# Optimization experiments

Measured on AMD Instinct MI355X. Metric: run time of the kernel, lower is better.

The kernel has to match this reference:

```python
import jax, jax.numpy as jnp
import numpy as np

N_NODES = 50000
N_EDGES = 600000
N_FEAT = 128
NHID = 128
N_CLASSES = 10
N_GRAPHS = 512
BN_EPS = 1e-5


def _gcn_conv(x, W, b, src, dst, n):
    """PyG GCNConv: D^{-1/2}(A+I)D^{-1/2} X W + b (symmetric norm, self-loops)."""
    xw = x @ W  # [n, out]
    deg = jax.ops.segment_sum(jnp.ones(src.shape[0], x.dtype), dst, num_segments=n) + 1.0
    dinv = jax.lax.rsqrt(deg)  # [n]
    norm = dinv[src] * dinv[dst]  # [E]
    agg = jax.ops.segment_sum(xw[src] * norm[:, None], dst, num_segments=n)
    agg = agg + xw * (dinv * dinv)[:, None]  # self-loop contribution
    return agg + b


def setup_inputs() -> dict:
    key = jax.random.key(0)
    ks = jax.random.split(key, 16)
    s_in = 1.0 / np.sqrt(N_FEAT)
    s_h = 1.0 / np.sqrt(NHID)
    s_h2 = 1.0 / np.sqrt(NHID // 2)
    return {
        "x": jax.random.normal(ks[0], (N_NODES, N_FEAT), jnp.float32),
        "edge_index": jax.random.randint(ks[1], (2, N_EDGES), 0, N_NODES, jnp.int32),
        "batch": jnp.sort(jax.random.randint(ks[2], (N_NODES,), 0, N_GRAPHS, jnp.int32)),
        "W1": jax.random.normal(ks[3], (N_FEAT, NHID), jnp.float32) * s_in,
        "b1": jnp.zeros((NHID,), jnp.float32),
        "W2": jax.random.normal(ks[4], (NHID, NHID), jnp.float32) * s_h,
        "b2": jnp.zeros((NHID,), jnp.float32),
        "W3": jax.random.normal(ks[5], (NHID, NHID), jnp.float32) * s_h,
        "b3": jnp.zeros((NHID,), jnp.float32),
        "gamma": jnp.ones((NHID,), jnp.float32),
        "beta": jnp.zeros((NHID,), jnp.float32),
        "run_mean": jnp.zeros((NHID,), jnp.float32),
        "run_var": jnp.ones((NHID,), jnp.float32),
        "lw1": jax.random.normal(ks[6], (NHID, NHID), jnp.float32) * s_h,
        "lb1": jnp.zeros((NHID,), jnp.float32),
        "lw2": jax.random.normal(ks[7], (NHID, NHID // 2), jnp.float32) * s_h,
        "lb2": jnp.zeros((NHID // 2,), jnp.float32),
        "lw3": jax.random.normal(ks[8], (NHID // 2, N_CLASSES), jnp.float32) * s_h2,
        "lb3": jnp.zeros((N_CLASSES,), jnp.float32),
    }


def reference(x, edge_index, batch, W1, b1, W2, b2, W3, b3,
              gamma, beta, run_mean, run_var,
              lw1, lb1, lw2, lb2, lw3, lb3):
    src, dst = edge_index[0], edge_index[1]
    h = jax.nn.relu(_gcn_conv(x, W1, b1, src, dst, N_NODES))
    h = jax.nn.relu(_gcn_conv(h, W2, b2, src, dst, N_NODES))
    h = jax.nn.relu(_gcn_conv(h, W3, b3, src, dst, N_NODES))
    # BatchNorm1d (eval: running stats)
    h = (h - run_mean) * jax.lax.rsqrt(run_var + BN_EPS) * gamma + beta
    # scatter_max over graph ids -> [N_GRAPHS, NHID]
    g = jax.ops.segment_max(h, batch, num_segments=N_GRAPHS)
    g = jax.nn.relu(g @ lw1 + lb1)
    g = jax.nn.relu(g @ lw2 + lb2)
    return g @ lw3 + lb3
```

## Files before the change

kernel.cpp:

```cpp
#include <hip/hip_runtime.h>
#include <hip/hip_bf16.h>

#define NHID 128
#define NGRAPH 512
#define NCLS 10

typedef __attribute__((ext_vector_type(8))) short bf16x8;
typedef __attribute__((ext_vector_type(4))) float f32x4;
typedef __attribute__((ext_vector_type(4))) unsigned int u32x4;

__device__ inline unsigned int fenc(float f) {
    unsigned int u = __float_as_uint(f);
    return (u & 0x80000000u) ? ~u : (u | 0x80000000u);
}
__device__ inline float fdec(unsigned int u) {
    u = (u & 0x80000000u) ? (u & 0x7fffffffu) : ~u;
    return __uint_as_float(u);
}
__device__ inline unsigned short f2bf(float f) {
    unsigned int u = __float_as_uint(f);
    return (unsigned short)((u + 0x7fffu + ((u >> 16) & 1u)) >> 16);
}
__device__ inline unsigned int packbf(float lo, float hi) {
    return (unsigned)f2bf(lo) | ((unsigned)f2bf(hi) << 16);
}

__global__ void k_deg(const int* __restrict__ dst, int* __restrict__ cnt, int E) {
    int e = blockIdx.x * blockDim.x + threadIdx.x;
    if (e < E) atomicAdd(&cnt[dst[e]], 1);
}

__global__ __launch_bounds__(1024) void k_scan1(const int* __restrict__ cnt,
        float* __restrict__ dinv, int* __restrict__ rowptr,
        int* __restrict__ bsum, int N) {
    __shared__ int lds[1024];
    int t = threadIdx.x;
    int i = blockIdx.x * 1024 + t;
    int v = (i < N) ? cnt[i] : 0;
    if (i < N) dinv[i] = rsqrtf((float)v + 1.0f);
    lds[t] = v;
    __syncthreads();
    for (int off = 1; off < 1024; off <<= 1) {
        int x = (t >= off) ? lds[t - off] : 0;
        __syncthreads();
        lds[t] += x;
        __syncthreads();
    }
    if (i < N) rowptr[i + 1] = lds[t];
    if (t == 1023) bsum[blockIdx.x] = lds[1023];
}

__global__ __launch_bounds__(1024) void k_scan2(int* __restrict__ bsum, int nb) {
    __shared__ int lds[1024];
    int t = threadIdx.x;
    int v = (t < nb) ? bsum[t] : 0;
    lds[t] = v;
    __syncthreads();
    for (int off = 1; off < 1024; off <<= 1) {
        int x = (t >= off) ? lds[t - off] : 0;
        __syncthreads();
        lds[t] += x;
        __syncthreads();
    }
    if (t < nb) bsum[t] = lds[t] - v;
}

__global__ void k_scan3(int* __restrict__ rowptr, const int* __restrict__ bsum, int N) {
    int i = blockIdx.x * 256 + threadIdx.x;
    if (i < N) rowptr[i + 1] += bsum[i >> 10];
    if (i == 0) rowptr[0] = 0;
}

__global__ void k_fill(const int* __restrict__ src, const int* __restrict__ dst,
                       const float* __restrict__ dinv, const int* __restrict__ rowptr,
                       int* __restrict__ cursor, int2* __restrict__ csr, int E) {
    int e = blockIdx.x * blockDim.x + threadIdx.x;
    if (e >= E) return;
    int s = src[e], d = dst[e];
    int pos = rowptr[d] + atomicAdd(&cursor[d], 1);
    csr[pos] = make_int2(s, __float_as_int(dinv[s] * dinv[d]));
}

__global__ void k_prep(const float* __restrict__ x, unsigned int* __restrict__ xb, int n8,
                       const float* __restrict__ W1, const float* __restrict__ W2,
                       const float* __restrict__ W3, unsigned short* __restrict__ Wt) {
    int i = blockIdx.x * 256 + threadIdx.x;
    if (i < n8) {
        const float* p = x + (size_t)i * 8;
        f32x4 a = *reinterpret_cast<const f32x4*>(p);
        f32x4 b = *reinterpret_cast<const f32x4*>(p + 4);
        u32x4 o;
        o[0] = packbf(a[0], a[1]);
        o[1] = packbf(a[2], a[3]);
        o[2] = packbf(b[0], b[1]);
        o[3] = packbf(b[2], b[3]);
        *reinterpret_cast<u32x4*>(xb + (size_t)i * 4) = o;
    } else {
        int idx = i - n8;
        if (idx < 3 * 16384) {
            int l = idx >> 14;
            int r = idx & 16383;
            const float* W = (l == 0) ? W1 : (l == 1) ? W2 : W3;
            int c = r & 127, k = r >> 7;
            Wt[l * 16384 + c * NHID + k] = f2bf(W[k * NHID + c]);
        }
    }
}

__device__ inline void fma8(const u32x4& u, float nw, float* a) {
#pragma unroll
    for (int q = 0; q < 4; ++q) {
        a[2 * q]     = fmaf(nw, __uint_as_float(u[q] << 16), a[2 * q]);
        a[2 * q + 1] = fmaf(nw, __uint_as_float(u[q] & 0xffff0000u), a[2 * q + 1]);
    }
}

__global__ __launch_bounds__(256) void k_agg(const unsigned int* __restrict__ Hb,
        const int2* __restrict__ csr, const int* __restrict__ rowptr,
        const float* __restrict__ dinv, unsigned int* __restrict__ aggb, int N) {
    int w = (blockIdx.x * 256 + threadIdx.x) >> 6;
    if (w >= N) return;
    int lane = threadIdx.x & 63;
    int g = lane >> 4;
    int l16 = lane & 15;
    float di = dinv[w];
    u32x4 us = reinterpret_cast<const u32x4*>(Hb + (size_t)w * (NHID / 2))[l16];
    float a[8];
#pragma unroll
    for (int e = 0; e < 8; ++e) a[e] = 0.f;
    int beg = rowptr[w], end = rowptr[w + 1];
    int trips = (end - beg + 15) >> 4;
    int j = beg + g;
    for (int t = 0; t < trips; ++t, j += 16) {
        int s0 = w, s1 = w, s2 = w, s3 = w;
        float n0 = 0.f, n1 = 0.f, n2 = 0.f, n3 = 0.f;
        if (j < end)      { int2 e2 = csr[j];      s0 = e2.x; n0 = __int_as_float(e2.y); }
        if (j + 4 < end)  { int2 e2 = csr[j + 4];  s1 = e2.x; n1 = __int_as_float(e2.y); }
        if (j + 8 < end)  { int2 e2 = csr[j + 8];  s2 = e2.x; n2 = __int_as_float(e2.y); }
        if (j + 12 < end) { int2 e2 = csr[j + 12]; s3 = e2.x; n3 = __int_as_float(e2.y); }
        u32x4 u0 = reinterpret_cast<const u32x4*>(Hb + (size_t)s0 * (NHID / 2))[l16];
        u32x4 u1 = reinterpret_cast<const u32x4*>(Hb + (size_t)s1 * (NHID / 2))[l16];
        u32x4 u2 = reinterpret_cast<const u32x4*>(Hb + (size_t)s2 * (NHID / 2))[l16];
        u32x4 u3 = reinterpret_cast<const u32x4*>(Hb + (size_t)s3 * (NHID / 2))[l16];
        fma8(u0, n0, a);
        fma8(u1, n1, a);
        fma8(u2, n2, a);
        fma8(u3, n3, a);
    }
    if (g == 0) fma8(us, di * di, a);
#pragma unroll
    for (int e = 0; e < 8; ++e) {
        a[e] += __shfl_xor(a[e], 16);
        a[e] += __shfl_xor(a[e], 32);
    }
    if (g == 0) {
        u32x4 o;
        o[0] = packbf(a[0], a[1]);
        o[1] = packbf(a[2], a[3]);
        o[2] = packbf(a[4], a[5]);
        o[3] = packbf(a[6], a[7]);
        *reinterpret_cast<u32x4*>(aggb + (size_t)w * (NHID / 2) + l16 * 4) = o;
    }
}

__global__ __launch_bounds__(256) void k_gemm(const unsigned short* __restrict__ A,
        const unsigned short* __restrict__ Wt, const float* __restrict__ bias,
        unsigned short* __restrict__ Hb, int M) {
    int wave = threadIdx.x >> 6;
    int lane = threadIdx.x & 63;
    int lr = lane & 15;
    int kq = lane >> 4;
    int r0 = blockIdx.x * 64 + wave * 16;
    f32x4 acc[8];
#pragma unroll
    for (int nt = 0; nt < 8; ++nt) acc[nt] = 0.f;
    int ar = r0 + lr;
    bool arok = ar < M;
#pragma unroll
    for (int kg = 0; kg < 4; ++kg) {
        int kb = kg * 32 + kq * 8;
        bf16x8 af = bf16x8(0);
        if (arok) af = *reinterpret_cast<const bf16x8*>(A + (size_t)ar * NHID + kb);
#pragma unroll
        for (int nt = 0; nt < 8; ++nt) {
            bf16x8 bf = *reinterpret_cast<const bf16x8*>(Wt + (size_t)(nt * 16 + lr) * NHID + kb);
            acc[nt] = __builtin_amdgcn_mfma_f32_16x16x32_bf16(af, bf, acc[nt], 0, 0, 0);
        }
    }
#pragma unroll
    for (int nt = 0; nt < 8; ++nt) {
        int c = nt * 16 + lr;
        float b = bias[c];
#pragma unroll
        for (int e = 0; e < 4; ++e) {
            int r = r0 + kq * 4 + e;
            if (r < M) {
                float v = fmaxf(acc[nt][e] + b, 0.f);
                Hb[(size_t)r * NHID + c] = f2bf(v);
            }
        }
    }
}

__global__ __launch_bounds__(256) void k_gemm_bn(const unsigned short* __restrict__ A,
        const unsigned short* __restrict__ Wt, const float* __restrict__ bias,
        const int* __restrict__ batch, const float* __restrict__ gamma,
        const float* __restrict__ beta, const float* __restrict__ rmean,
        const float* __restrict__ rvar, unsigned int* __restrict__ keys, int M) {
    __shared__ unsigned int smax[64][NHID];
    __shared__ int bseg[64];
    int tid = threadIdx.x;
    int n0 = blockIdx.x * 64;
    for (int i = tid; i < 64 * NHID; i += 256) ((unsigned int*)smax)[i] = 0u;
    if (tid < 64) {
        int r = n0 + tid;
        bseg[tid] = batch[r < M ? r : M - 1];
    }
    int wave = tid >> 6;
    int lane = tid & 63;
    int lr = lane & 15;
    int kq = lane >> 4;
    int r0 = n0 + wave * 16;
    f32x4 acc[8];
#pragma unroll
    for (int nt = 0; nt < 8; ++nt) acc[nt] = 0.f;
    int ar = r0 + lr;
    bool arok = ar < M;
#pragma unroll
    for (int kg = 0; kg < 4; ++kg) {
        int kb = kg * 32 + kq * 8;
        bf16x8 af = bf16x8(0);
        if (arok) af = *reinterpret_cast<const bf16x8*>(A + (size_t)ar * NHID + kb);
#pragma unroll
        for (int nt = 0; nt < 8; ++nt) {
            bf16x8 bf = *reinterpret_cast<const bf16x8*>(Wt + (size_t)(nt * 16 + lr) * NHID + kb);
            acc[nt] = __builtin_amdgcn_mfma_f32_16x16x32_bf16(af, bf, acc[nt], 0, 0, 0);
        }
    }
    __syncthreads();
    int glo = bseg[0];
#pragma unroll
    for (int nt = 0; nt < 8; ++nt) {
        int c = nt * 16 + lr;
        float b = bias[c];
        float sc = gamma[c] * rsqrtf(rvar[c] + 1e-5f);
        float sh = beta[c] - rmean[c] * sc;
#pragma unroll
        for (int e = 0; e < 4; ++e) {
            int rr = wave * 16 + kq * 4 + e;
            if (n0 + rr < M) {
                float v = fmaxf(acc[nt][e] + b, 0.f);
                float y = fmaf(v, sc, sh);
                atomicMax(&smax[bseg[rr] - glo][c], fenc(y));
            }
        }
    }
    __syncthreads();
    int last = M - 1 - n0;
    if (last > 63) last = 63;
    int span = bseg[last] - glo + 1;
    for (int i = tid; i < span * NHID; i += 256) {
        unsigned int v = ((unsigned int*)smax)[i];
        if (v) atomicMax(&keys[(size_t)(glo + (i >> 7)) * NHID + (i & 127)], v);
    }
}

__global__ __launch_bounds__(128) void k_head(const unsigned int* __restrict__ keys,
        const float* __restrict__ lw1, const float* __restrict__ lb1,
        const float* __restrict__ lw2, const float* __restrict__ lb2,
        const float* __restrict__ lw3, const float* __restrict__ lb3,
        float* __restrict__ out) {
    __shared__ float g0[NHID], g1[NHID], g2[64];
    int r = blockIdx.x;
    int t = threadIdx.x;
    unsigned int u = keys[(size_t)r * NHID + t];
    g0[t] = (u == 0u) ? -3.0e38f : fdec(u);
    __syncthreads();
    float acc = lb1[t];
#pragma unroll 8
    for (int k = 0; k < NHID; ++k) acc = fmaf(g0[k], lw1[k * NHID + t], acc);
    g1[t] = fmaxf(acc, 0.f);
    __syncthreads();
    if (t < 64) {
        acc = lb2[t];
#pragma unroll 8
        for (int k = 0; k < NHID; ++k) acc = fmaf(g1[k], lw2[k * 64 + t], acc);
        g2[t] = fmaxf(acc, 0.f);
    }
    __syncthreads();
    if (t < NCLS) {
        acc = lb3[t];
#pragma unroll 8
        for (int k = 0; k < 64; ++k) acc = fmaf(g2[k], lw3[k * NCLS + t], acc);
        out[(size_t)r * NCLS + t] = acc;
    }
}

extern "C" void kernel_launch(void* const* d_in, const int* in_sizes, int n_in,
                              void* d_out, int out_size, void* d_ws, size_t ws_size,
                              hipStream_t stream) {
    const float* x     = (const float*)d_in[0];
    const int*   ei    = (const int*)d_in[1];
    const int*   batch = (const int*)d_in[2];
    const float* W1 = (const float*)d_in[3];
    const float* b1 = (const float*)d_in[4];
    const float* W2 = (const float*)d_in[5];
    const float* b2 = (const float*)d_in[6];
    const float* W3 = (const float*)d_in[7];
    const float* b3 = (const float*)d_in[8];
    const float* gamma = (const float*)d_in[9];
    const float* beta  = (const float*)d_in[10];
    const float* rmean = (const float*)d_in[11];
    const float* rvar  = (const float*)d_in[12];
    const float* lw1 = (const float*)d_in[13];
    const float* lb1 = (const float*)d_in[14];
    const float* lw2 = (const float*)d_in[15];
    const float* lb2 = (const float*)d_in[16];
    const float* lw3 = (const float*)d_in[17];
    const float* lb3 = (const float*)d_in[18];

    const int N = in_sizes[2];
    const int E = in_sizes[1] / 2;
    const int* src = ei;
    const int* dst = ei + E;

    char* ws = (char*)d_ws;
    size_t off = 0;
    auto alloc = [&](size_t bytes) {
        char* p = ws + off;
        off += (bytes + 255) & ~(size_t)255;
        return p;
    };
    int*   cnt     = (int*)  alloc((size_t)N * 8);
    int*   cursor  = cnt + N;
    int*   rowptr  = (int*)  alloc(((size_t)N + 1) * 4);
    int*   bsum    = (int*)  alloc(1024 * 4);
    float* dinv    = (float*)alloc((size_t)N * 4);
    int2*  csr     = (int2*) alloc((size_t)E * 8);
    unsigned int* xb   = (unsigned int*)alloc((size_t)N * NHID * 2);
    unsigned int* aggb = (unsigned int*)alloc((size_t)N * NHID * 2);
    unsigned int* Hb   = (unsigned int*)alloc((size_t)N * NHID * 2);
    unsigned short* Wt = (unsigned short*)alloc((size_t)3 * NHID * NHID * 2);
    unsigned int* keys = (unsigned int*)alloc((size_t)NGRAPH * NHID * 4);
    (void)ws_size; (void)n_in; (void)out_size;

    hipMemsetAsync(cnt, 0, (size_t)N * 8, stream);
    hipMemsetAsync(keys, 0, (size_t)NGRAPH * NHID * 4, stream);

    int eb = (E + 255) / 256;
    int nb1 = (N + 1023) / 1024;
    k_deg<<<eb, 256, 0, stream>>>(dst, cnt, E);
    k_scan1<<<nb1, 1024, 0, stream>>>(cnt, dinv, rowptr, bsum, N);
    k_scan2<<<1, 1024, 0, stream>>>(bsum, nb1);
    k_scan3<<<(N + 255) / 256, 256, 0, stream>>>(rowptr, bsum, N);
    k_fill<<<eb, 256, 0, stream>>>(src, dst, dinv, rowptr, cursor, csr, E);
    int n8 = N * 16;
    k_prep<<<(n8 + 3 * 16384 + 255) / 256, 256, 0, stream>>>(x, xb, n8, W1, W2, W3, Wt);

    int ab = ((size_t)N * 64 + 255) / 256;
    int gb = (N + 63) / 64;
    k_agg<<<ab, 256, 0, stream>>>(xb, csr, rowptr, dinv, aggb, N);
    k_gemm<<<gb, 256, 0, stream>>>((const unsigned short*)aggb, Wt, b1, (unsigned short*)Hb, N);
    k_agg<<<ab, 256, 0, stream>>>(Hb, csr, rowptr, dinv, aggb, N);
    k_gemm<<<gb, 256, 0, stream>>>((const unsigned short*)aggb, Wt + 16384, b2, (unsigned short*)Hb, N);
    k_agg<<<ab, 256, 0, stream>>>(Hb, csr, rowptr, dinv, aggb, N);
    k_gemm_bn<<<gb, 256, 0, stream>>>((const unsigned short*)aggb, Wt + 32768, b3,
                                      batch, gamma, beta, rmean, rvar, keys, N);

    k_head<<<NGRAPH, 128, 0, stream>>>(keys, lw1, lb1, lw2, lb2, lw3, lb3, (float*)d_out);
}
```

Baseline: 249.3 us.

## Split aggregation into feature partitions and fuse front-end prep kernels

Aggregation now splits the 128 features into four 32-feature partitions, each handled by a separate block group. Within a partition a lane loads 4 bytes per edge instead of 16, and blocks are 1024 threads. The goal is better cache locality: each pass gathers a narrower column slice of H, so the working set that must stay in L2/MALL shrinks. The degree count, x bf16 conversion, weight transpose and keys zeroing are merged into one launch, and the separate scan3 pass is removed by adding the block offset at use sites. In exchange, the CSR is re-read four times and loop and index overhead repeats per partition.

```diff
diff --git a/kernel.cpp b/kernel.cpp
--- a/kernel.cpp
+++ b/kernel.cpp
@@ -24,10 +24,42 @@
 __device__ inline unsigned int packbf(float lo, float hi) {
     return (unsigned)f2bf(lo) | ((unsigned)f2bf(hi) << 16);
 }
-
-__global__ void k_deg(const int* __restrict__ dst, int* __restrict__ cnt, int E) {
-    int e = blockIdx.x * blockDim.x + threadIdx.x;
-    if (e < E) atomicAdd(&cnt[dst[e]], 1);
+__device__ inline float bflo(unsigned int u) { return __uint_as_float(u << 16); }
+__device__ inline float bfhi(unsigned int u) { return __uint_as_float(u & 0xffff0000u); }
+
+__global__ void k_front(const int* __restrict__ dst, int* __restrict__ cnt, int E, int degB,
+                        const float* __restrict__ x, unsigned int* __restrict__ xb, int n8, int xB,
+                        const float* __restrict__ W1, const float* __restrict__ W2,
+                        const float* __restrict__ W3, unsigned short* __restrict__ Wt,
+                        unsigned int* __restrict__ keys) {
+    int b = blockIdx.x;
+    if (b < degB) {
+        int e = b * 256 + threadIdx.x;
+        if (e < E) atomicAdd(&cnt[dst[e]], 1);
+    } else if (b < degB + xB) {
+        int i = (b - degB) * 256 + threadIdx.x;
+        if (i < n8) {
+            const float* p = x + (size_t)i * 8;
+            f32x4 a = *reinterpret_cast<const f32x4*>(p);
+            f32x4 c = *reinterpret_cast<const f32x4*>(p + 4);
+            u32x4 o;
+            o[0] = packbf(a[0], a[1]);
+            o[1] = packbf(a[2], a[3]);
+            o[2] = packbf(c[0], c[1]);
+            o[3] = packbf(c[2], c[3]);
+            *reinterpret_cast<u32x4*>(xb + (size_t)i * 4) = o;
+        }
+    } else if (b < degB + xB + 192) {
+        int idx = (b - degB - xB) * 256 + threadIdx.x;
+        int l = idx >> 14;
+        int r = idx & 16383;
+        const float* W = (l == 0) ? W1 : (l == 1) ? W2 : W3;
+        int c = r & 127, k = r >> 7;
+        Wt[l * 16384 + c * NHID + k] = f2bf(W[k * NHID + c]);
+    } else {
+        int i = (b - degB - xB - 192) * 256 + threadIdx.x;
+        if (i < NGRAPH * NHID) keys[i] = 0u;
+    }
 }
 
 __global__ __launch_bounds__(1024) void k_scan1(const int* __restrict__ cnt,
@@ -46,7 +78,7 @@
         lds[t] += x;
         __syncthreads();
     }
-    if (i < N) rowptr[i + 1] = lds[t];
+    if (i < N) rowptr[i] = lds[t] - v;
     if (t == 1023) bsum[blockIdx.x] = lds[1023];
 }
 
@@ -65,71 +97,37 @@
     if (t < nb) bsum[t] = lds[t] - v;
 }
 
-__global__ void k_scan3(int* __restrict__ rowptr, const int* __restrict__ bsum, int N) {
-    int i = blockIdx.x * 256 + threadIdx.x;
-    if (i < N) rowptr[i + 1] += bsum[i >> 10];
-    if (i == 0) rowptr[0] = 0;
-}
-
 __global__ void k_fill(const int* __restrict__ src, const int* __restrict__ dst,
                        const float* __restrict__ dinv, const int* __restrict__ rowptr,
-                       int* __restrict__ cursor, int2* __restrict__ csr, int E) {
+                       const int* __restrict__ bsum, int* __restrict__ cursor,
+                       int2* __restrict__ csr, int E) {
     int e = blockIdx.x * blockDim.x + threadIdx.x;
     if (e >= E) return;
     int s = src[e], d = dst[e];
-    int pos = rowptr[d] + atomicAdd(&cursor[d], 1);
+    int pos = rowptr[d] + bsum[d >> 10] + atomicAdd(&cursor[d], 1);
     csr[pos] = make_int2(s, __float_as_int(dinv[s] * dinv[d]));
 }
 
-__global__ void k_prep(const float* __restrict__ x, unsigned int* __restrict__ xb, int n8,
-                       const float* __restrict__ W1, const float* __restrict__ W2,
-                       const float* __restrict__ W3, unsigned short* __restrict__ Wt) {
-    int i = blockIdx.x * 256 + threadIdx.x;
-    if (i < n8) {
-        const float* p = x + (size_t)i * 8;
-        f32x4 a = *reinterpret_cast<const f32x4*>(p);
-        f32x4 b = *reinterpret_cast<const f32x4*>(p + 4);
-        u32x4 o;
-        o[0] = packbf(a[0], a[1]);
-        o[1] = packbf(a[2], a[3]);
-        o[2] = packbf(b[0], b[1]);
-        o[3] = packbf(b[2], b[3]);
-        *reinterpret_cast<u32x4*>(xb + (size_t)i * 4) = o;
-    } else {
-        int idx = i - n8;
-        if (idx < 3 * 16384) {
-            int l = idx >> 14;
-            int r = idx & 16383;
-            const float* W = (l == 0) ? W1 : (l == 1) ? W2 : W3;
-            int c = r & 127, k = r >> 7;
-            Wt[l * 16384 + c * NHID + k] = f2bf(W[k * NHID + c]);
-        }
-    }
-}
-
-__device__ inline void fma8(const u32x4& u, float nw, float* a) {
-#pragma unroll
-    for (int q = 0; q < 4; ++q) {
-        a[2 * q]     = fmaf(nw, __uint_as_float(u[q] << 16), a[2 * q]);
-        a[2 * q + 1] = fmaf(nw, __uint_as_float(u[q] & 0xffff0000u), a[2 * q + 1]);
-    }
-}
-
-__global__ __launch_bounds__(256) void k_agg(const unsigned int* __restrict__ Hb,
+__global__ __launch_bounds__(1024) void k_aggp(const unsigned int* __restrict__ H32,
         const int2* __restrict__ csr, const int* __restrict__ rowptr,
-        const float* __restrict__ dinv, unsigned int* __restrict__ aggb, int N) {
-    int w = (blockIdx.x * 256 + threadIdx.x) >> 6;
+        const int* __restrict__ bsum, const int* __restrict__ cnt,
+        const float* __restrict__ dinv, unsigned int* __restrict__ aggb,
+        int N, int nbp) {
+    int p = blockIdx.x / nbp;
+    int nb = blockIdx.x - p * nbp;
+    int w = nb * 16 + (threadIdx.x >> 6);
     if (w >= N) return;
     int lane = threadIdx.x & 63;
     int g = lane >> 4;
     int l16 = lane & 15;
+    int co = p * 16 + l16;
+    int beg = rowptr[w] + bsum[w >> 10];
+    int deg = cnt[w];
+    int end = beg + deg;
     float di = dinv[w];
-    u32x4 us = reinterpret_cast<const u32x4*>(Hb + (size_t)w * (NHID / 2))[l16];
-    float a[8];
-#pragma unroll
-    for (int e = 0; e < 8; ++e) a[e] = 0.f;
-    int beg = rowptr[w], end = rowptr[w + 1];
-    int trips = (end - beg + 15) >> 4;
+    unsigned int us = H32[(size_t)w * 64 + co];
+    float a0 = 0.f, a1 = 0.f;
+    int trips = (deg + 15) >> 4;
     int j = beg + g;
     for (int t = 0; t < trips; ++t, j += 16) {
         int s0 = w, s1 = w, s2 = w, s3 = w;
@@ -138,29 +136,22 @@
         if (j + 4 < end)  { int2 e2 = csr[j + 4];  s1 = e2.x; n1 = __int_as_float(e2.y); }
         if (j + 8 < end)  { int2 e2 = csr[j + 8];  s2 = e2.x; n2 = __int_as_float(e2.y); }
         if (j + 12 < end) { int2 e2 = csr[j + 12]; s3 = e2.x; n3 = __int_as_float(e2.y); }
-        u32x4 u0 = reinterpret_cast<const u32x4*>(Hb + (size_t)s0 * (NHID / 2))[l16];
-        u32x4 u1 = reinterpret_cast<const u32x4*>(Hb + (size_t)s1 * (NHID / 2))[l16];
-        u32x4 u2 = reinterpret_cast<const u32x4*>(Hb + (size_t)s2 * (NHID / 2))[l16];
-        u32x4 u3 = reinterpret_cast<const u32x4*>(Hb + (size_t)s3 * (NHID / 2))[l16];
-        fma8(u0, n0, a);
-        fma8(u1, n1, a);
-        fma8(u2, n2, a);
-        fma8(u3, n3, a);
-    }
-    if (g == 0) fma8(us, di * di, a);
-#pragma unroll
-    for (int e = 0; e < 8; ++e) {
-        a[e] += __shfl_xor(a[e], 16);
-        a[e] += __shfl_xor(a[e], 32);
+        unsigned int u0 = H32[(size_t)s0 * 64 + co];
+        unsigned int u1 = H32[(size_t)s1 * 64 + co];
+        unsigned int u2 = H32[(size_t)s2 * 64 + co];
+        unsigned int u3 = H32[(size_t)s3 * 64 + co];
+        a0 = fmaf(n0, bflo(u0), a0); a1 = fmaf(n0, bfhi(u0), a1);
+        a0 = fmaf(n1, bflo(u1), a0); a1 = fmaf(n1, bfhi(u1), a1);
+        a0 = fmaf(n2, bflo(u2), a0); a1 = fmaf(n2, bfhi(u2), a1);
+        a0 = fmaf(n3, bflo(u3), a0); a1 = fmaf(n3, bfhi(u3), a1);
     }
     if (g == 0) {
-        u32x4 o;
-        o[0] = packbf(a[0], a[1]);
-        o[1] = packbf(a[2], a[3]);
-        o[2] = packbf(a[4], a[5]);
-        o[3] = packbf(a[6], a[7]);
-        *reinterpret_cast<u32x4*>(aggb + (size_t)w * (NHID / 2) + l16 * 4) = o;
-    }
+        a0 = fmaf(di * di, bflo(us), a0);
+        a1 = fmaf(di * di, bfhi(us), a1);
+    }
+    a0 += __shfl_xor(a0, 16); a0 += __shfl_xor(a0, 32);
+    a1 += __shfl_xor(a1, 16); a1 += __shfl_xor(a1, 32);
+    if (g == 0) aggb[(size_t)w * 64 + co] = packbf(a0, a1);
 }
 
 __global__ __launch_bounds__(256) void k_gemm(const unsigned short* __restrict__ A,
@@ -333,7 +324,7 @@
     };
     int*   cnt     = (int*)  alloc((size_t)N * 8);
     int*   cursor  = cnt + N;
-    int*   rowptr  = (int*)  alloc(((size_t)N + 1) * 4);
+    int*   rowptr  = (int*)  alloc((size_t)N * 4);
     int*   bsum    = (int*)  alloc(1024 * 4);
     float* dinv    = (float*)alloc((size_t)N * 4);
     int2*  csr     = (int2*) alloc((size_t)E * 8);
@@ -345,25 +336,26 @@
     (void)ws_size; (void)n_in; (void)out_size;
 
     hipMemsetAsync(cnt, 0, (size_t)N * 8, stream);
-    hipMemsetAsync(keys, 0, (size_t)NGRAPH * NHID * 4, stream);
-
-    int eb = (E + 255) / 256;
+
+    int degB = (E + 255) / 256;
+    int n8 = N * 16;
+    int xB = (n8 + 255) / 256;
+    int frontB = degB + xB + 192 + (NGRAPH * NHID + 255) / 256;
+    k_front<<<frontB, 256, 0, stream>>>(dst, cnt, E, degB, x, xb, n8, xB,
+                                        W1, W2, W3, Wt, keys);
     int nb1 = (N + 1023) / 1024;
-    k_deg<<<eb, 256, 0, stream>>>(dst, cnt, E);
     k_scan1<<<nb1, 1024, 0, stream>>>(cnt, dinv, rowptr, bsum, N);
     k_scan2<<<1, 1024, 0, stream>>>(bsum, nb1);
-    k_scan3<<<(N + 255) / 256, 256, 0, stream>>>(rowptr, bsum, N);
-    k_fill<<<eb, 256, 0, stream>>>(src, dst, dinv, rowptr, cursor, csr, E);
-    int n8 = N * 16;
-    k_prep<<<(n8 + 3 * 16384 + 255) / 256, 256, 0, stream>>>(x, xb, n8, W1, W2, W3, Wt);
-
-    int ab = ((size_t)N * 64 + 255) / 256;
+    k_fill<<<degB, 256, 0, stream>>>(src, dst, dinv, rowptr, bsum, cursor, csr, E);
+
+    int nbp = (N + 15) / 16;
+    int agrid = 4 * nbp;
     int gb = (N + 63) / 64;
-    k_agg<<<ab, 256, 0, stream>>>(xb, csr, rowptr, dinv, aggb, N);
+    k_aggp<<<agrid, 1024, 0, stream>>>(xb, csr, rowptr, bsum, cnt, dinv, aggb, N, nbp);
     k_gemm<<<gb, 256, 0, stream>>>((const unsigned short*)aggb, Wt, b1, (unsigned short*)Hb, N);
-    k_agg<<<ab, 256, 0, stream>>>(Hb, csr, rowptr, dinv, aggb, N);
+    k_aggp<<<agrid, 1024, 0, stream>>>(Hb, csr, rowptr, bsum, cnt, dinv, aggb, N, nbp);
     k_gemm<<<gb, 256, 0, stream>>>((const unsigned short*)aggb, Wt + 16384, b2, (unsigned short*)Hb, N);
-    k_agg<<<ab, 256, 0, stream>>>(Hb, csr, rowptr, dinv, aggb, N);
+    k_aggp<<<agrid, 1024, 0, stream>>>(Hb, csr, rowptr, bsum, cnt, dinv, aggb, N, nbp);
     k_gemm_bn<<<gb, 256, 0, stream>>>((const unsigned short*)aggb, Wt + 32768, b3,
                                       batch, gamma, beta, rmean, rvar, keys, N);
 
```

Result: slower. 408.3 us (+63.8%).

## Merge front-end kernels, drop scan3, store CSR as source indices only

Applied to the files above, without the earlier changes.

Degree counting, x-to-bf16 conversion, weight transposition and key zeroing now run in one multi-role launch, replacing two kernels and a memset. The final scan-add kernel is removed: rowptr holds block-local exclusive prefixes, and consumers add the block offset and read the degree from cnt. The CSR keeps only source indices, and aggregation computes the norm from dinv on the fly. This halves CSR traffic and cuts launch count, at the cost of an extra dinv gather per edge in each of the three aggregations.

```diff
diff --git a/kernel.cpp b/kernel.cpp
--- a/kernel.cpp
+++ b/kernel.cpp
@@ -25,9 +25,39 @@
     return (unsigned)f2bf(lo) | ((unsigned)f2bf(hi) << 16);
 }
 
-__global__ void k_deg(const int* __restrict__ dst, int* __restrict__ cnt, int E) {
-    int e = blockIdx.x * blockDim.x + threadIdx.x;
-    if (e < E) atomicAdd(&cnt[dst[e]], 1);
+__global__ void k_front(const int* __restrict__ dst, int* __restrict__ cnt, int E, int degB,
+                        const float* __restrict__ x, unsigned int* __restrict__ xb, int n8, int xB,
+                        const float* __restrict__ W1, const float* __restrict__ W2,
+                        const float* __restrict__ W3, unsigned short* __restrict__ Wt,
+                        unsigned int* __restrict__ keys) {
+    int b = blockIdx.x;
+    if (b < degB) {
+        int e = b * 256 + threadIdx.x;
+        if (e < E) atomicAdd(&cnt[dst[e]], 1);
+    } else if (b < degB + xB) {
+        int i = (b - degB) * 256 + threadIdx.x;
+        if (i < n8) {
+            const float* p = x + (size_t)i * 8;
+            f32x4 a = *reinterpret_cast<const f32x4*>(p);
+            f32x4 c = *reinterpret_cast<const f32x4*>(p + 4);
+            u32x4 o;
+            o[0] = packbf(a[0], a[1]);
+            o[1] = packbf(a[2], a[3]);
+            o[2] = packbf(c[0], c[1]);
+            o[3] = packbf(c[2], c[3]);
+            *reinterpret_cast<u32x4*>(xb + (size_t)i * 4) = o;
+        }
+    } else if (b < degB + xB + 192) {
+        int idx = (b - degB - xB) * 256 + threadIdx.x;
+        int l = idx >> 14;
+        int r = idx & 16383;
+        const float* W = (l == 0) ? W1 : (l == 1) ? W2 : W3;
+        int c = r & 127, k = r >> 7;
+        Wt[l * 16384 + c * NHID + k] = f2bf(W[k * NHID + c]);
+    } else {
+        int i = (b - degB - xB - 192) * 256 + threadIdx.x;
+        if (i < NGRAPH * NHID) keys[i] = 0u;
+    }
 }
 
 __global__ __launch_bounds__(1024) void k_scan1(const int* __restrict__ cnt,
@@ -46,7 +76,7 @@
         lds[t] += x;
         __syncthreads();
     }
-    if (i < N) rowptr[i + 1] = lds[t];
+    if (i < N) rowptr[i] = lds[t] - v;
     if (t == 1023) bsum[blockIdx.x] = lds[1023];
 }
 
@@ -65,46 +95,14 @@
     if (t < nb) bsum[t] = lds[t] - v;
 }
 
-__global__ void k_scan3(int* __restrict__ rowptr, const int* __restrict__ bsum, int N) {
-    int i = blockIdx.x * 256 + threadIdx.x;
-    if (i < N) rowptr[i + 1] += bsum[i >> 10];
-    if (i == 0) rowptr[0] = 0;
-}
-
 __global__ void k_fill(const int* __restrict__ src, const int* __restrict__ dst,
-                       const float* __restrict__ dinv, const int* __restrict__ rowptr,
-                       int* __restrict__ cursor, int2* __restrict__ csr, int E) {
+                       const int* __restrict__ rowptr, const int* __restrict__ bsum,
+                       int* __restrict__ cursor, int* __restrict__ csr_src, int E) {
     int e = blockIdx.x * blockDim.x + threadIdx.x;
     if (e >= E) return;
     int s = src[e], d = dst[e];
-    int pos = rowptr[d] + atomicAdd(&cursor[d], 1);
-    csr[pos] = make_int2(s, __float_as_int(dinv[s] * dinv[d]));
-}
-
-__global__ void k_prep(const float* __restrict__ x, unsigned int* __restrict__ xb, int n8,
-                       const float* __restrict__ W1, const float* __restrict__ W2,
-                       const float* __restrict__ W3, unsigned short* __restrict__ Wt) {
-    int i = blockIdx.x * 256 + threadIdx.x;
-    if (i < n8) {
-        const float* p = x + (size_t)i * 8;
-        f32x4 a = *reinterpret_cast<const f32x4*>(p);
-        f32x4 b = *reinterpret_cast<const f32x4*>(p + 4);
-        u32x4 o;
-        o[0] = packbf(a[0], a[1]);
-        o[1] = packbf(a[2], a[3]);
-        o[2] = packbf(b[0], b[1]);
-        o[3] = packbf(b[2], b[3]);
-        *reinterpret_cast<u32x4*>(xb + (size_t)i * 4) = o;
-    } else {
-        int idx = i - n8;
-        if (idx < 3 * 16384) {
-            int l = idx >> 14;
-            int r = idx & 16383;
-            const float* W = (l == 0) ? W1 : (l == 1) ? W2 : W3;
-            int c = r & 127, k = r >> 7;
-            Wt[l * 16384 + c * NHID + k] = f2bf(W[k * NHID + c]);
-        }
-    }
+    int pos = rowptr[d] + bsum[d >> 10] + atomicAdd(&cursor[d], 1);
+    csr_src[pos] = s;
 }
 
 __device__ inline void fma8(const u32x4& u, float nw, float* a) {
@@ -116,28 +114,34 @@
 }
 
 __global__ __launch_bounds__(256) void k_agg(const unsigned int* __restrict__ Hb,
-        const int2* __restrict__ csr, const int* __restrict__ rowptr,
+        const int* __restrict__ csr_src, const int* __restrict__ rowptr,
+        const int* __restrict__ bsum, const int* __restrict__ cnt,
         const float* __restrict__ dinv, unsigned int* __restrict__ aggb, int N) {
     int w = (blockIdx.x * 256 + threadIdx.x) >> 6;
     if (w >= N) return;
     int lane = threadIdx.x & 63;
     int g = lane >> 4;
     int l16 = lane & 15;
-    float di = dinv[w];
+    float diw = dinv[w];
     u32x4 us = reinterpret_cast<const u32x4*>(Hb + (size_t)w * (NHID / 2))[l16];
     float a[8];
 #pragma unroll
     for (int e = 0; e < 8; ++e) a[e] = 0.f;
-    int beg = rowptr[w], end = rowptr[w + 1];
-    int trips = (end - beg + 15) >> 4;
+    int beg = rowptr[w] + bsum[w >> 10];
+    int deg = cnt[w];
+    int end = beg + deg;
+    int trips = (deg + 15) >> 4;
     int j = beg + g;
     for (int t = 0; t < trips; ++t, j += 16) {
         int s0 = w, s1 = w, s2 = w, s3 = w;
-        float n0 = 0.f, n1 = 0.f, n2 = 0.f, n3 = 0.f;
-        if (j < end)      { int2 e2 = csr[j];      s0 = e2.x; n0 = __int_as_float(e2.y); }
-        if (j + 4 < end)  { int2 e2 = csr[j + 4];  s1 = e2.x; n1 = __int_as_float(e2.y); }
-        if (j + 8 < end)  { int2 e2 = csr[j + 8];  s2 = e2.x; n2 = __int_as_float(e2.y); }
-        if (j + 12 < end) { int2 e2 = csr[j + 12]; s3 = e2.x; n3 = __int_as_float(e2.y); }
+        if (j < end)      s0 = csr_src[j];
+        if (j + 4 < end)  s1 = csr_src[j + 4];
+        if (j + 8 < end)  s2 = csr_src[j + 8];
+        if (j + 12 < end) s3 = csr_src[j + 12];
+        float n0 = (j < end)      ? dinv[s0] * diw : 0.f;
+        float n1 = (j + 4 < end)  ? dinv[s1] * diw : 0.f;
+        float n2 = (j + 8 < end)  ? dinv[s2] * diw : 0.f;
+        float n3 = (j + 12 < end) ? dinv[s3] * diw : 0.f;
         u32x4 u0 = reinterpret_cast<const u32x4*>(Hb + (size_t)s0 * (NHID / 2))[l16];
         u32x4 u1 = reinterpret_cast<const u32x4*>(Hb + (size_t)s1 * (NHID / 2))[l16];
         u32x4 u2 = reinterpret_cast<const u32x4*>(Hb + (size_t)s2 * (NHID / 2))[l16];
@@ -147,7 +151,7 @@
         fma8(u2, n2, a);
         fma8(u3, n3, a);
     }
-    if (g == 0) fma8(us, di * di, a);
+    if (g == 0) fma8(us, diw * diw, a);
 #pragma unroll
     for (int e = 0; e < 8; ++e) {
         a[e] += __shfl_xor(a[e], 16);
@@ -333,10 +337,10 @@
     };
     int*   cnt     = (int*)  alloc((size_t)N * 8);
     int*   cursor  = cnt + N;
-    int*   rowptr  = (int*)  alloc(((size_t)N + 1) * 4);
+    int*   rowptr  = (int*)  alloc((size_t)N * 4);
     int*   bsum    = (int*)  alloc(1024 * 4);
     float* dinv    = (float*)alloc((size_t)N * 4);
-    int2*  csr     = (int2*) alloc((size_t)E * 8);
+    int*   csr_src = (int*)  alloc((size_t)E * 4);
     unsigned int* xb   = (unsigned int*)alloc((size_t)N * NHID * 2);
     unsigned int* aggb = (unsigned int*)alloc((size_t)N * NHID * 2);
     unsigned int* Hb   = (unsigned int*)alloc((size_t)N * NHID * 2);
@@ -345,25 +349,25 @@
     (void)ws_size; (void)n_in; (void)out_size;
 
     hipMemsetAsync(cnt, 0, (size_t)N * 8, stream);
-    hipMemsetAsync(keys, 0, (size_t)NGRAPH * NHID * 4, stream);
-
-    int eb = (E + 255) / 256;
+
+    int degB = (E + 255) / 256;
+    int n8 = N * 16;
+    int xB = (n8 + 255) / 256;
+    int frontB = degB + xB + 192 + (NGRAPH * NHID + 255) / 256;
+    k_front<<<frontB, 256, 0, stream>>>(dst, cnt, E, degB, x, xb, n8, xB,
+                                        W1, W2, W3, Wt, keys);
     int nb1 = (N + 1023) / 1024;
-    k_deg<<<eb, 256, 0, stream>>>(dst, cnt, E);
     k_scan1<<<nb1, 1024, 0, stream>>>(cnt, dinv, rowptr, bsum, N);
     k_scan2<<<1, 1024, 0, stream>>>(bsum, nb1);
-    k_scan3<<<(N + 255) / 256, 256, 0, stream>>>(rowptr, bsum, N);
-    k_fill<<<eb, 256, 0, stream>>>(src, dst, dinv, rowptr, cursor, csr, E);
-    int n8 = N * 16;
-    k_prep<<<(n8 + 3 * 16384 + 255) / 256, 256, 0, stream>>>(x, xb, n8, W1, W2, W3, Wt);
+    k_fill<<<degB, 256, 0, stream>>>(src, dst, rowptr, bsum, cursor, csr_src, E);
 
     int ab = ((size_t)N * 64 + 255) / 256;
     int gb = (N + 63) / 64;
-    k_agg<<<ab, 256, 0, stream>>>(xb, csr, rowptr, dinv, aggb, N);
+    k_agg<<<ab, 256, 0, stream>>>(xb, csr_src, rowptr, bsum, cnt, dinv, aggb, N);
     k_gemm<<<gb, 256, 0, stream>>>((const unsigned short*)aggb, Wt, b1, (unsigned short*)Hb, N);
-    k_agg<<<ab, 256, 0, stream>>>(Hb, csr, rowptr, dinv, aggb, N);
+    k_agg<<<ab, 256, 0, stream>>>(Hb, csr_src, rowptr, bsum, cnt, dinv, aggb, N);
     k_gemm<<<gb, 256, 0, stream>>>((const unsigned short*)aggb, Wt + 16384, b2, (unsigned short*)Hb, N);
-    k_agg<<<ab, 256, 0, stream>>>(Hb, csr, rowptr, dinv, aggb, N);
+    k_agg<<<ab, 256, 0, stream>>>(Hb, csr_src, rowptr, bsum, cnt, dinv, aggb, N);
     k_gemm_bn<<<gb, 256, 0, stream>>>((const unsigned short*)aggb, Wt + 32768, b3,
                                       batch, gamma, beta, rmean, rvar, keys, N);
 
```

New measurement: 248.9 us. No clear change (-0.2%).
